# Performance work log

Measured on AMD Instinct MI355X. Metric: run time of the kernel, lower is better.

Reference implementation:

```python
import jax, jax.numpy as jnp
import numpy as np

MUL = 128            # multiplicity of every irrep (128x0e node features)
LS = (0, 1, 2, 3)    # sh irreps 0e,1o,2e,3o
SH_DIMS = tuple(2 * l + 1 for l in LS)  # (1,3,5,7) -> total 16
RB = 8               # radial basis features
N_NODES, N_EDGES = 5000, 100000


def setup_inputs() -> dict:
    key = jax.random.key(0)
    ks = jax.random.split(key, 12)
    return {
        "node_features": jax.random.normal(ks[0], (N_NODES, MUL), jnp.float32),
        "sph_harmonics": jax.random.normal(ks[1], (N_EDGES, sum(SH_DIMS)), jnp.float32),
        "radial_basis": jax.random.uniform(ks[2], (N_EDGES, RB), jnp.float32),
        "edge_i": jax.random.randint(ks[3], (N_EDGES,), 0, N_NODES),  # central atoms
        "edge_j": jax.random.randint(ks[4], (N_EDGES,), 0, N_NODES),  # neighbours
        "W_pre": jax.random.normal(ks[5], (MUL, MUL), jnp.float32),
        "mlp_w0": jax.random.normal(ks[6], (RB, 64), jnp.float32),
        "mlp_w1": jax.random.normal(ks[7], (64, 64), jnp.float32),
        "mlp_w2": jax.random.normal(ks[8], (64, 64), jnp.float32),
        "mlp_w3": jax.random.normal(ks[9], (64, len(LS) * MUL), jnp.float32),
        "W_post": jax.random.normal(ks[10], (len(LS), MUL, MUL), jnp.float32),
    }


def _forward(node_features, sph, rb, edge_i, edge_j,
             W_pre, mlp_w0, mlp_w1, mlp_w2, mlp_w3, W_post):
    N = node_features.shape[0]
    inv = np.float32(1.0 / np.sqrt(MUL))
    # pre o3.Linear on 128x0e: dense mix of multiplicities, fan-in normalized
    x = (node_features @ W_pre) * inv                       # [N, MUL]
    nbr = x[edge_j]                                         # gather neighbours [E, MUL]
    # per-edge weight generator: SiLU hidden layers, linear last, no bias
    h = rb
    for w in (mlp_w0, mlp_w1, mlp_w2):
        h = jax.nn.silu((h @ w) * np.float32(1.0 / np.sqrt(w.shape[0])))
    w_edge = (h @ mlp_w3) * np.float32(1.0 / np.sqrt(mlp_w3.shape[0]))  # [E, 4*MUL]
    w_edge = w_edge.reshape(-1, len(LS), MUL)               # one weight chunk per CG path
    off = 0
    out_blocks = []
    for p, d in enumerate(SH_DIMS):
        Y = sph[:, off:off + d]; off += d                   # [E, d]
        m = (nbr * w_edge[:, p, :])[:, :, None] * Y[:, None, :]  # messages [E, MUL, d]
        # scatter-aggregate messages onto central atoms (sum aggregation)
        tot = jax.ops.segment_sum(m.reshape(m.shape[0], -1), edge_i, num_segments=N)
        tot = tot.reshape(N, MUL, d)
        # post o3.Linear: per-irrep dense mix of multiplicities
        out_blocks.append(jnp.einsum('nud,uv->nvd', tot, W_post[p]) * inv)
    # reshape_irreps: [N, MUL, 1+3+5+7] = [N, 128, 16]
    return jnp.concatenate(out_blocks, axis=-1)


def reference(node_features, sph_harmonics, radial_basis, edge_i, edge_j,
              W_pre, mlp_w0, mlp_w1, mlp_w2, mlp_w3, W_post):
    return _forward(node_features, sph_harmonics, radial_basis, edge_i, edge_j,
                    W_pre, mlp_w0, mlp_w1, mlp_w2, mlp_w3, W_post)
```

## Files before the change

kernel.cpp:

```cpp
#include <hip/hip_runtime.h>
#include <hip/hip_bf16.h>

#define NN 5000
#define NE 100000

typedef unsigned short u16;
typedef __attribute__((ext_vector_type(8))) short bf16x8;
typedef __attribute__((ext_vector_type(8))) unsigned short u16x8;
typedef __attribute__((ext_vector_type(4))) float f32x4;

__device__ __forceinline__ float silu_f(float x) {
    return x / (1.0f + __expf(-x));
}

__device__ __forceinline__ u16 f2bf(float x) {
    unsigned int u = __float_as_uint(x);
    u += 0x7FFFu + ((u >> 16) & 1u);
    return (u16)(u >> 16);
}
__device__ __forceinline__ float bf2f(u16 h) {
    return __uint_as_float(((unsigned int)h) << 16);
}

__global__ __launch_bounds__(128) void k_pre(const float* __restrict__ nf,
                                             const float* __restrict__ Wpre,
                                             float* __restrict__ x) {
    __shared__ float row[128];
    int n = blockIdx.x;
    int v = threadIdx.x;
    row[v] = nf[(size_t)n * 128 + v];
    __syncthreads();
    float acc = 0.f;
#pragma unroll 16
    for (int u = 0; u < 128; ++u) acc += row[u] * Wpre[u * 128 + v];
    x[(size_t)n * 128 + v] = acc * 0.08838834764831845f;
}

__global__ void k_count(const int* __restrict__ ei, int* __restrict__ counts) {
    int e = blockIdx.x * blockDim.x + threadIdx.x;
    if (e < NE) atomicAdd(&counts[ei[e]], 1);
}

__global__ __launch_bounds__(256) void k_scan(const int* __restrict__ counts,
                                              int* __restrict__ offsets) {
    __shared__ int part[256];
    int t = threadIdx.x;
    const int CH = 20;
    int lo = t * CH, hi = min(lo + CH, NN);
    int s = 0;
    for (int i = lo; i < hi; ++i) s += counts[i];
    part[t] = s;
    __syncthreads();
    if (t == 0) {
        int run = 0;
        for (int i = 0; i < 256; ++i) { int v = part[i]; part[i] = run; run += v; }
    }
    __syncthreads();
    int run = part[t];
    for (int i = lo; i < hi; ++i) { offsets[i] = run; run += counts[i]; }
    if (t == 0) offsets[NN] = NE;
}

__global__ void k_fill(const int* __restrict__ ei, const int* __restrict__ offsets,
                       int* __restrict__ cursor, int* __restrict__ order) {
    int e = blockIdx.x * blockDim.x + threadIdx.x;
    if (e < NE) {
        int i = ei[e];
        int pos = atomicAdd(&cursor[i], 1);
        order[offsets[i] + pos] = e;
    }
}

__global__ __launch_bounds__(256) void k_wprep(const float* __restrict__ w1,
                                               const float* __restrict__ w2,
                                               const float* __restrict__ w3,
                                               u16* __restrict__ w1h, u16* __restrict__ w1l,
                                               u16* __restrict__ w2h, u16* __restrict__ w2l,
                                               u16* __restrict__ w3h, u16* __restrict__ w3l) {
    int i = blockIdx.x * 256 + threadIdx.x;
    if (i < 4096) {
        int k = i >> 6, n = i & 63;
        float v = w1[i];
        u16 h = f2bf(v), l = f2bf(v - bf2f(h));
        w1h[n * 64 + k] = h; w1l[n * 64 + k] = l;
        v = w2[i];
        h = f2bf(v); l = f2bf(v - bf2f(h));
        w2h[n * 64 + k] = h; w2l[n * 64 + k] = l;
    }
    if (i < 32768) {
        int k = i >> 9, n = i & 511;
        float v = w3[i];
        u16 h = f2bf(v), l = f2bf(v - bf2f(h));
        w3h[n * 64 + k] = h; w3l[n * 64 + k] = l;
    }
}

__global__ __launch_bounds__(256) void k_wpprep(const float* __restrict__ Wpost,
                                                u16* __restrict__ wpth,
                                                u16* __restrict__ wptl) {
    int i = blockIdx.x * 256 + threadIdx.x;
    int p = i >> 14, rem = i & 16383, u = rem >> 7, v = rem & 127;
    float val = Wpost[i];
    u16 h = f2bf(val), l = f2bf(val - bf2f(h));
    int o = (p * 128 + v) * 128 + u;
    wpth[o] = h; wptl[o] = l;
}

__device__ __forceinline__ void layer_mid(const char* s,
                                          const u16* __restrict__ wh,
                                          const u16* __restrict__ wl,
                                          char* d, int w, int l) {
    const int col = w * 16 + (l & 15);
    bf16x8 Bh[2], Bl[2];
#pragma unroll
    for (int kc = 0; kc < 2; ++kc) {
        Bh[kc] = *(const bf16x8*)(wh + col * 64 + kc * 32 + ((l >> 4) << 3));
        Bl[kc] = *(const bf16x8*)(wl + col * 64 + kc * 32 + ((l >> 4) << 3));
    }
#pragma unroll
    for (int rt = 0; rt < 4; ++rt) {
        const int arow = rt * 16 + (l & 15);
        f32x4 acc = {0.f, 0.f, 0.f, 0.f};
#pragma unroll
        for (int kc = 0; kc < 2; ++kc) {
            int off = (arow * 128 + kc * 64 + ((l >> 4) << 4)) ^ ((arow & 7) << 4);
            bf16x8 a = *(const bf16x8*)(s + off);
            acc = __builtin_amdgcn_mfma_f32_16x16x32_bf16(a, Bh[kc], acc, 0, 0, 0);
            acc = __builtin_amdgcn_mfma_f32_16x16x32_bf16(a, Bl[kc], acc, 0, 0, 0);
        }
#pragma unroll
        for (int r = 0; r < 4; ++r) {
            float v = silu_f(acc[r] * 0.125f);
            int orow = rt * 16 + ((l >> 4) << 2) + r;
            int off = (orow * 128 + col * 2) ^ ((orow & 7) << 4);
            *(u16*)(d + off) = f2bf(v);
        }
    }
}

__device__ __forceinline__ void layer_out(const char* s,
                                          const u16* __restrict__ wh,
                                          const u16* __restrict__ wl,
                                          u16* __restrict__ we, int base, int w, int l) {
    const int r0 = (w & 1) * 32;
    const int c0 = (w >> 1) * 256;
    bf16x8 A[2][2];
#pragma unroll
    for (int rt = 0; rt < 2; ++rt)
#pragma unroll
        for (int kc = 0; kc < 2; ++kc) {
            int row = r0 + rt * 16 + (l & 15);
            int off = (row * 128 + kc * 64 + ((l >> 4) << 4)) ^ ((row & 7) << 4);
            A[rt][kc] = *(const bf16x8*)(s + off);
        }
    for (int nt = 0; nt < 16; ++nt) {
        const int col = c0 + nt * 16 + (l & 15);
        f32x4 acc[2] = {{0.f, 0.f, 0.f, 0.f}, {0.f, 0.f, 0.f, 0.f}};
#pragma unroll
        for (int kc = 0; kc < 2; ++kc) {
            bf16x8 bh = *(const bf16x8*)(wh + col * 64 + kc * 32 + ((l >> 4) << 3));
            bf16x8 bl = *(const bf16x8*)(wl + col * 64 + kc * 32 + ((l >> 4) << 3));
#pragma unroll
            for (int rt = 0; rt < 2; ++rt) {
                acc[rt] = __builtin_amdgcn_mfma_f32_16x16x32_bf16(A[rt][kc], bh, acc[rt], 0, 0, 0);
                acc[rt] = __builtin_amdgcn_mfma_f32_16x16x32_bf16(A[rt][kc], bl, acc[rt], 0, 0, 0);
            }
        }
        const int up = ((col & 127) << 2) + (col >> 7);
#pragma unroll
        for (int rt = 0; rt < 2; ++rt)
#pragma unroll
            for (int r = 0; r < 4; ++r) {
                int row = r0 + rt * 16 + ((l >> 4) << 2) + r;
                int e = base + row;
                if (e < NE) we[(size_t)e * 512 + up] = f2bf(acc[rt][r] * 0.125f);
            }
    }
}

__global__ __launch_bounds__(256) void k_mlp(const float* __restrict__ rb,
                                             const float* __restrict__ w0,
                                             const u16* __restrict__ w1h, const u16* __restrict__ w1l,
                                             const u16* __restrict__ w2h, const u16* __restrict__ w2l,
                                             const u16* __restrict__ w3h, const u16* __restrict__ w3l,
                                             u16* __restrict__ we) {
    __shared__ __align__(16) char hA[8192];
    __shared__ __align__(16) char hB[8192];
    __shared__ float rbs[512];
    const int t = threadIdx.x;
    const int l = t & 63, w = t >> 6;
    const int base = blockIdx.x * 64;

    for (int i = t; i < 512; i += 256) {
        int e = base + (i >> 3);
        rbs[i] = (e < NE) ? rb[(size_t)e * 8 + (i & 7)] : 0.f;
    }
    __syncthreads();

    {
        const int m = t >> 2, n0 = (t & 3) * 16;
        float h[16];
#pragma unroll
        for (int nn = 0; nn < 16; ++nn) h[nn] = 0.f;
#pragma unroll
        for (int k = 0; k < 8; ++k) {
            float r = rbs[m * 8 + k];
            const float* wp = w0 + k * 64 + n0;
#pragma unroll
            for (int nn = 0; nn < 16; ++nn) h[nn] += r * wp[nn];
        }
#pragma unroll
        for (int nn = 0; nn < 16; ++nn) {
            float v = silu_f(h[nn] * 0.35355339059327373f);
            int off = (m * 128 + (n0 + nn) * 2) ^ ((m & 7) << 4);
            *(u16*)(hA + off) = f2bf(v);
        }
    }
    __syncthreads();
    layer_mid(hA, w1h, w1l, hB, w, l);
    __syncthreads();
    layer_mid(hB, w2h, w2l, hA, w, l);
    __syncthreads();
    layer_out(hA, w3h, w3l, we, base, w, l);
}

__global__ __launch_bounds__(256) void k_gather(const float* __restrict__ x,
                                                const u16* __restrict__ we,
                                                const float* __restrict__ sph,
                                                const int* __restrict__ ej,
                                                const int* __restrict__ offsets,
                                                const int* __restrict__ order,
                                                u16* __restrict__ toth,
                                                u16* __restrict__ totl) {
    const int lane = threadIdx.x & 63;
    const int n = blockIdx.x * 4 + (threadIdx.x >> 6);
    if (n >= NN) return;
    const int s0 = offsets[n], s1 = offsets[n + 1];

    float acc0[16] = {};
    float acc1[16] = {};
    const int PMAP[16] = {0,1,1,1, 2,2,2,2, 2,3,3,3, 3,3,3,3};

    for (int base = s0; base < s1; base += 64) {
        int idx = base + lane;
        int ev = (idx < s1) ? order[idx] : 0;
        int jv = (idx < s1) ? ej[ev] : 0;
        int cnt = min(64, s1 - base);
        for (int i = 0; i < cnt; ++i) {
            int e = __shfl(ev, i);
            int j = __shfl(jv, i);
            const float* xp = x + (size_t)j * 128;
            float xj0 = xp[lane];
            float xj1 = xp[lane + 64];
            const u16* wep = we + (size_t)e * 512;
            ushort4 w0v = *(const ushort4*)(wep + lane * 4);
            ushort4 w1v = *(const ushort4*)(wep + (lane + 64) * 4);
            float a0[4] = {xj0 * bf2f(w0v.x), xj0 * bf2f(w0v.y),
                           xj0 * bf2f(w0v.z), xj0 * bf2f(w0v.w)};
            float a1[4] = {xj1 * bf2f(w1v.x), xj1 * bf2f(w1v.y),
                           xj1 * bf2f(w1v.z), xj1 * bf2f(w1v.w)};
            const float4* Y4 = (const float4*)(sph + (size_t)e * 16);
            float yv[16];
            ((float4*)yv)[0] = Y4[0];
            ((float4*)yv)[1] = Y4[1];
            ((float4*)yv)[2] = Y4[2];
            ((float4*)yv)[3] = Y4[3];
#pragma unroll
            for (int k = 0; k < 16; ++k) {
                acc0[k] += a0[PMAP[k]] * yv[k];
                acc1[k] += a1[PMAP[k]] * yv[k];
            }
        }
    }

#pragma unroll
    for (int k = 0; k < 16; ++k) {
        size_t o = ((size_t)n * 16 + k) * 128;
        u16 h0 = f2bf(acc0[k]);
        toth[o + lane] = h0;
        totl[o + lane] = f2bf(acc0[k] - bf2f(h0));
        u16 h1 = f2bf(acc1[k]);
        toth[o + 64 + lane] = h1;
        totl[o + 64 + lane] = f2bf(acc1[k] - bf2f(h1));
    }
}

__global__ __launch_bounds__(256) void k_post(const u16* __restrict__ toth,
                                              const u16* __restrict__ totl,
                                              const u16* __restrict__ wpth,
                                              const u16* __restrict__ wptl,
                                              float* __restrict__ out) {
    __shared__ __align__(16) u16 tot_h[4][2176];
    __shared__ __align__(16) u16 tot_l[4][2176];
    __shared__ __align__(16) float stage[4][4][16][16];
    const int lane = threadIdx.x & 63;
    const int wv = threadIdx.x >> 6;
    const int n0 = blockIdx.x * 4;

    for (int i = threadIdx.x; i < 1024; i += 256) {
        int nb = i >> 8;
        int rem = i & 255;
        int k = rem >> 4, u8 = (rem & 15) << 3;
        size_t g = (size_t)(n0 + nb) * 2048 + rem * 8;
        *(u16x8*)&tot_h[nb][k * 136 + u8] = *(const u16x8*)(toth + g);
        *(u16x8*)&tot_l[nb][k * 136 + u8] = *(const u16x8*)(totl + g);
    }
    __syncthreads();

    const int l15 = lane & 15, lg = lane >> 4;
    const int KSTART[4] = {0, 1, 4, 9};
    const int DP[4]     = {1, 3, 5, 7};
    const float inv = 0.08838834764831845f;

    for (int vi = 0; vi < 2; ++vi) {
        const int vt = wv * 2 + vi;
        for (int p = 0; p < 4; ++p) {
            const int kst = KSTART[p];
            int kr = kst + l15; if (kr > 15) kr = 15;
            f32x4 acc[4] = {{0,0,0,0},{0,0,0,0},{0,0,0,0},{0,0,0,0}};
#pragma unroll
            for (int ks = 0; ks < 4; ++ks) {
                size_t aoff = ((size_t)(p * 128 + vt * 16 + l15)) * 128 + ks * 32 + lg * 8;
                bf16x8 Ah = *(const bf16x8*)(wpth + aoff);
                bf16x8 Al = *(const bf16x8*)(wptl + aoff);
                int bidx = kr * 136 + ks * 32 + lg * 8;
#pragma unroll
                for (int nb = 0; nb < 4; ++nb) {
                    bf16x8 Bh = *(const bf16x8*)(&tot_h[nb][bidx]);
                    bf16x8 Bl = *(const bf16x8*)(&tot_l[nb][bidx]);
                    acc[nb] = __builtin_amdgcn_mfma_f32_16x16x32_bf16(Ah, Bh, acc[nb], 0, 0, 0);
                    acc[nb] = __builtin_amdgcn_mfma_f32_16x16x32_bf16(Ah, Bl, acc[nb], 0, 0, 0);
                    acc[nb] = __builtin_amdgcn_mfma_f32_16x16x32_bf16(Al, Bh, acc[nb], 0, 0, 0);
                }
            }
            if (l15 < DP[p]) {
                const int kg = kst + l15;
#pragma unroll
                for (int nb = 0; nb < 4; ++nb)
#pragma unroll
                    for (int r = 0; r < 4; ++r)
                        stage[wv][nb][lg * 4 + r][kg] = acc[nb][r] * inv;
            }
        }
        __syncthreads();
#pragma unroll
        for (int nb = 0; nb < 4; ++nb) {
            const float4 vle = *(const float4*)&stage[wv][nb][lane >> 2][(lane & 3) * 4];
            *(float4*)&out[(size_t)(n0 + nb) * 2048 + vt * 256 + (lane >> 2) * 16 + (lane & 3) * 4] = vle;
        }
        __syncthreads();
    }
}

extern "C" void kernel_launch(void* const* d_in, const int* in_sizes, int n_in,
                              void* d_out, int out_size, void* d_ws, size_t ws_size,
                              hipStream_t stream) {
    const float* nf    = (const float*)d_in[0];
    const float* sph   = (const float*)d_in[1];
    const float* rb    = (const float*)d_in[2];
    const int*   ei    = (const int*)d_in[3];
    const int*   ej    = (const int*)d_in[4];
    const float* Wpre  = (const float*)d_in[5];
    const float* w0    = (const float*)d_in[6];
    const float* w1    = (const float*)d_in[7];
    const float* w2    = (const float*)d_in[8];
    const float* w3    = (const float*)d_in[9];
    const float* Wpost = (const float*)d_in[10];
    float* out = (float*)d_out;

    char* ws = (char*)d_ws;
    const size_t OFF_X       = 0;
    const size_t OFF_WE      = 2560000;
    const size_t OFF_COUNTS  = 104960000;
    const size_t OFF_CURSOR  = 104980000;
    const size_t OFF_OFFSETS = 105000000;
    const size_t OFF_ORDER   = 105020032;
    const size_t OFF_W1H     = 105420032;
    const size_t OFF_W1L     = OFF_W1H + 8192;
    const size_t OFF_W2H     = OFF_W1L + 8192;
    const size_t OFF_W2L     = OFF_W2H + 8192;
    const size_t OFF_W3H     = OFF_W2L + 8192;
    const size_t OFF_W3L     = OFF_W3H + 65536;
    const size_t OFF_WPTH    = OFF_W3L + 65536;
    const size_t OFF_WPTL    = OFF_WPTH + 131072;
    const size_t OFF_TOTH    = OFF_WPTL + 131072;
    const size_t OFF_TOTL    = OFF_TOTH + 20480000;
    const size_t NEEDED      = OFF_TOTL + 20480000;
    if (ws_size < NEEDED) return;

    float* x       = (float*)(ws + OFF_X);
    u16*   we      = (u16*)(ws + OFF_WE);
    int*   counts  = (int*)(ws + OFF_COUNTS);
    int*   cursor  = (int*)(ws + OFF_CURSOR);
    int*   offsets = (int*)(ws + OFF_OFFSETS);
    int*   order   = (int*)(ws + OFF_ORDER);
    u16*   w1h = (u16*)(ws + OFF_W1H); u16* w1l = (u16*)(ws + OFF_W1L);
    u16*   w2h = (u16*)(ws + OFF_W2H); u16* w2l = (u16*)(ws + OFF_W2L);
    u16*   w3h = (u16*)(ws + OFF_W3H); u16* w3l = (u16*)(ws + OFF_W3L);
    u16*   wpth = (u16*)(ws + OFF_WPTH);
    u16*   wptl = (u16*)(ws + OFF_WPTL);
    u16*   toth = (u16*)(ws + OFF_TOTH);
    u16*   totl = (u16*)(ws + OFF_TOTL);

    (void)hipMemsetAsync(ws + OFF_COUNTS, 0, 40000, stream);

    k_count<<<(NE + 255) / 256, 256, 0, stream>>>(ei, counts);
    k_scan<<<1, 256, 0, stream>>>(counts, offsets);
    k_fill<<<(NE + 255) / 256, 256, 0, stream>>>(ei, offsets, cursor, order);
    k_wprep<<<128, 256, 0, stream>>>(w1, w2, w3, w1h, w1l, w2h, w2l, w3h, w3l);
    k_wpprep<<<256, 256, 0, stream>>>(Wpost, wpth, wptl);

    k_pre<<<NN, 128, 0, stream>>>(nf, Wpre, x);
    k_mlp<<<(NE + 63) / 64, 256, 0, stream>>>(rb, w0, w1h, w1l, w2h, w2l, w3h, w3l, we);
    k_gather<<<(NN + 3) / 4, 256, 0, stream>>>(x, we, sph, ej, offsets, order, toth, totl);
    k_post<<<NN / 4, 256, 0, stream>>>(toth, totl, wpth, wptl, out);
}
```

Before: 274.5 us.

## Stage edge-weight output through LDS for coalesced stores and path-major layout

The last MLP layer now writes its bf16 results into a shared-memory staging buffer, padded to a 520-element row stride and aliased over the earlier activation buffers, instead of scattering 2-byte stores to global memory. It then copies whole rows out with 16-byte vector stores. The per-edge weight layout also changes from channel-interleaved (u*4+p) to path-major (p*128+u), and the gather kernel now reads four coalesced 2-byte loads per lane instead of two ushort4 loads. The aim is to cut uncoalesced store traffic in the MLP. The cost is extra barriers, an accumulator set split into two halves, and narrower loads in the gather.

New measurement: 307.4 us. +12.0%, slower.

```diff
diff --git a/kernel.cpp b/kernel.cpp
--- a/kernel.cpp
+++ b/kernel.cpp
@@ -141,40 +141,53 @@
 __device__ __forceinline__ void layer_out(const char* s,
                                           const u16* __restrict__ wh,
                                           const u16* __restrict__ wl,
+                                          u16* __restrict__ stage,
                                           u16* __restrict__ we, int base, int w, int l) {
     const int r0 = (w & 1) * 32;
     const int c0 = (w >> 1) * 256;
+    const int l15 = l & 15, lg = l >> 4;
     bf16x8 A[2][2];
 #pragma unroll
     for (int rt = 0; rt < 2; ++rt)
 #pragma unroll
         for (int kc = 0; kc < 2; ++kc) {
-            int row = r0 + rt * 16 + (l & 15);
-            int off = (row * 128 + kc * 64 + ((l >> 4) << 4)) ^ ((row & 7) << 4);
+            int row = r0 + rt * 16 + l15;
+            int off = (row * 128 + kc * 64 + (lg << 4)) ^ ((row & 7) << 4);
             A[rt][kc] = *(const bf16x8*)(s + off);
         }
-    for (int nt = 0; nt < 16; ++nt) {
-        const int col = c0 + nt * 16 + (l & 15);
-        f32x4 acc[2] = {{0.f, 0.f, 0.f, 0.f}, {0.f, 0.f, 0.f, 0.f}};
-#pragma unroll
-        for (int kc = 0; kc < 2; ++kc) {
-            bf16x8 bh = *(const bf16x8*)(wh + col * 64 + kc * 32 + ((l >> 4) << 3));
-            bf16x8 bl = *(const bf16x8*)(wl + col * 64 + kc * 32 + ((l >> 4) << 3));
-#pragma unroll
-            for (int rt = 0; rt < 2; ++rt) {
-                acc[rt] = __builtin_amdgcn_mfma_f32_16x16x32_bf16(A[rt][kc], bh, acc[rt], 0, 0, 0);
-                acc[rt] = __builtin_amdgcn_mfma_f32_16x16x32_bf16(A[rt][kc], bl, acc[rt], 0, 0, 0);
-            }
-        }
-        const int up = ((col & 127) << 2) + (col >> 7);
-#pragma unroll
-        for (int rt = 0; rt < 2; ++rt)
+    __syncthreads();
+
+#pragma unroll
+    for (int half = 0; half < 2; ++half) {
+        for (int nt = 0; nt < 16; ++nt) {
+            const int col = c0 + nt * 16 + l15;
+            f32x4 acc = {0.f, 0.f, 0.f, 0.f};
+#pragma unroll
+            for (int kc = 0; kc < 2; ++kc) {
+                bf16x8 bh = *(const bf16x8*)(wh + col * 64 + kc * 32 + (lg << 3));
+                bf16x8 bl = *(const bf16x8*)(wl + col * 64 + kc * 32 + (lg << 3));
+                acc = __builtin_amdgcn_mfma_f32_16x16x32_bf16(A[half][kc], bh, acc, 0, 0, 0);
+                acc = __builtin_amdgcn_mfma_f32_16x16x32_bf16(A[half][kc], bl, acc, 0, 0, 0);
+            }
 #pragma unroll
             for (int r = 0; r < 4; ++r) {
-                int row = r0 + rt * 16 + ((l >> 4) << 2) + r;
-                int e = base + row;
-                if (e < NE) we[(size_t)e * 512 + up] = f2bf(acc[rt][r] * 0.125f);
-            }
+                int slot = (w & 1) * 16 + lg * 4 + r;
+                stage[slot * 520 + col] = f2bf(acc[r] * 0.125f);
+            }
+        }
+        __syncthreads();
+        const int tid = w * 64 + l;
+#pragma unroll
+        for (int it = 0; it < 8; ++it) {
+            int i = tid + it * 256;
+            int slot = i >> 6, chunk = i & 63;
+            int el = (slot & 15) + ((slot >> 4) * 32) + half * 16;
+            int e = base + el;
+            if (e < NE)
+                *(u16x8*)(we + (size_t)e * 512 + chunk * 8) =
+                    *(const u16x8*)(stage + slot * 520 + chunk * 8);
+        }
+        __syncthreads();
     }
 }
 
@@ -184,9 +197,11 @@
                                              const u16* __restrict__ w2h, const u16* __restrict__ w2l,
                                              const u16* __restrict__ w3h, const u16* __restrict__ w3l,
                                              u16* __restrict__ we) {
-    __shared__ __align__(16) char hA[8192];
-    __shared__ __align__(16) char hB[8192];
-    __shared__ float rbs[512];
+    __shared__ __align__(16) char smem[33280];
+    char*  hA    = smem;
+    char*  hB    = smem + 8192;
+    float* rbs   = (float*)(smem + 16384);
+    u16*   stage = (u16*)smem;
     const int t = threadIdx.x;
     const int l = t & 63, w = t >> 6;
     const int base = blockIdx.x * 64;
@@ -221,7 +236,7 @@
     __syncthreads();
     layer_mid(hB, w2h, w2l, hA, w, l);
     __syncthreads();
-    layer_out(hA, w3h, w3l, we, base, w, l);
+    layer_out(hA, w3h, w3l, stage, we, base, w, l);
 }
 
 __global__ __launch_bounds__(256) void k_gather(const float* __restrict__ x,
@@ -253,12 +268,12 @@
             float xj0 = xp[lane];
             float xj1 = xp[lane + 64];
             const u16* wep = we + (size_t)e * 512;
-            ushort4 w0v = *(const ushort4*)(wep + lane * 4);
-            ushort4 w1v = *(const ushort4*)(wep + (lane + 64) * 4);
-            float a0[4] = {xj0 * bf2f(w0v.x), xj0 * bf2f(w0v.y),
-                           xj0 * bf2f(w0v.z), xj0 * bf2f(w0v.w)};
-            float a1[4] = {xj1 * bf2f(w1v.x), xj1 * bf2f(w1v.y),
-                           xj1 * bf2f(w1v.z), xj1 * bf2f(w1v.w)};
+            float a0[4], a1[4];
+#pragma unroll
+            for (int p = 0; p < 4; ++p) {
+                a0[p] = xj0 * bf2f(wep[p * 128 + lane]);
+                a1[p] = xj1 * bf2f(wep[p * 128 + 64 + lane]);
+            }
             const float4* Y4 = (const float4*)(sph + (size_t)e * 16);
             float yv[16];
             ((float4*)yv)[0] = Y4[0];
```
